# Kernel optimization log

Hardware: AMD Instinct MI355X
Metric: run time of the kernel (lower is better)

The kernel has to match this reference:

```python
import jax, jax.numpy as jnp
import numpy as np

K = 256  # number of leaf nodes in the cluster tree


def setup_inputs() -> dict:
    key = jax.random.key(0)
    k1, k2 = jax.random.split(key)
    minibatch = jax.random.normal(k1, (131072, 64), dtype=jnp.float32)
    centers = jax.random.normal(k2, (K, 64), dtype=jnp.float32)
    return {"minibatch": minibatch, "centers": centers}


def reference(minibatch, centers):
    # Euclidean cdist (p=2) between samples [N,D] and leaf centers [K,D]
    x_sq = jnp.sum(minibatch * minibatch, axis=1, keepdims=True)      # [N,1]
    c_sq = jnp.sum(centers * centers, axis=1)[None, :]                # [1,K]
    dist_sq = x_sq + c_sq - 2.0 * (minibatch @ centers.T)             # [N,K]
    dist_sq = jnp.maximum(dist_sq, 0.0)
    dist = jnp.sqrt(dist_sq)

    # nearest-leaf routing (torch.min over dim=1)
    assignments = jnp.argmin(dist, axis=1)                            # [N] int
    min_dists = jnp.min(dist, axis=1)                                 # [N]

    # per-leaf statistics (vectorized form of the per-node assignment loop):
    # counts -> node.assignments length, sums -> analytic center updates,
    # sum_sq -> node.sum_squared_dist
    ones = jnp.ones(minibatch.shape[0], dtype=minibatch.dtype)
    leaf_counts = jax.ops.segment_sum(ones, assignments, num_segments=K)           # [K]
    leaf_sums = jax.ops.segment_sum(minibatch, assignments, num_segments=K)        # [K,D]
    leaf_sum_sq_dist = jax.ops.segment_sum(min_dists * min_dists, assignments,
                                           num_segments=K)                         # [K]
    return assignments, min_dists, leaf_counts, leaf_sums, leaf_sum_sq_dist
```

## Files before the change

kernel.cpp:

```cpp
#include <hip/hip_runtime.h>
#include <float.h>

#define NS 131072
#define DD 64
#define KK 256
#define CPAD 72
#define NSTAT 16896
#define XTS 264
#define XTSW 132
#define NCOPY 512
#define RGROUPS 16
#define RPER 32
#define P_OFF_F ((size_t)NCOPY * NSTAT)
#define P_CSQ_F 9216
#define P_IMG_I4 2304

typedef __attribute__((ext_vector_type(8))) short bf16x8;
typedef __attribute__((ext_vector_type(4))) float f32x4;
typedef __attribute__((ext_vector_type(4))) unsigned int u32x4;


__global__ void zero_buf(float* __restrict__ p, int n) {
    int i = blockIdx.x * 256 + threadIdx.x;
    if (i < n) p[i] = 0.f;
}

__device__ inline unsigned short f2bf(float f) {
    unsigned u = __float_as_uint(f);
    u += 0x7FFFu + ((u >> 16) & 1u);
    return (unsigned short)(u >> 16);
}
__device__ inline float bf2f(unsigned short b) {
    return __uint_as_float(((unsigned)b) << 16);
}

__global__ void prep_centers(const float* __restrict__ ctr, float* __restrict__ P) {
    __shared__ float s_part[32][9];
    const int t = threadIdx.x;
    const int rl = t >> 3, seg = t & 7;
    const int r = blockIdx.x * 32 + rl;
    const float* rp = ctr + r * DD + seg * 8;
    float4 a = ((const float4*)rp)[0];
    float4 b = ((const float4*)rp)[1];
    unsigned short u0 = f2bf(a.x), u1 = f2bf(a.y), u2 = f2bf(a.z), u3 = f2bf(a.w);
    unsigned short u4 = f2bf(b.x), u5 = f2bf(b.y), u6 = f2bf(b.z), u7 = f2bf(b.w);
    float q0 = bf2f(u0), q1 = bf2f(u1), q2 = bf2f(u2), q3 = bf2f(u3);
    float q4 = bf2f(u4), q5 = bf2f(u5), q6 = bf2f(u6), q7 = bf2f(u7);
    float p = (q0*q0 + q1*q1 + q2*q2 + q3*q3) + (q4*q4 + q5*q5 + q6*q6 + q7*q7);

    unsigned short* Pu = (unsigned short*)P;
    int4 pack;
    pack.x = (int)((unsigned)u0 | ((unsigned)u1 << 16));
    pack.y = (int)((unsigned)u2 | ((unsigned)u3 << 16));
    pack.z = (int)((unsigned)u4 | ((unsigned)u5 << 16));
    pack.w = (int)((unsigned)u6 | ((unsigned)u7 << 16));
    *(int4*)(Pu + (size_t)r * CPAD + seg * 8) = pack;
    if (seg == 0) {
        int4 z; z.x = 0; z.y = 0; z.z = 0; z.w = 0;
        *(int4*)(Pu + (size_t)r * CPAD + 64) = z;
    }
    s_part[rl][seg] = p;
    __syncthreads();
    if (seg == 0) {
        float s = 0.f;
        #pragma unroll
        for (int k = 0; k < 8; ++k) s += s_part[rl][k];
        P[P_CSQ_F + r] = s;
    }
}

__global__ void reduce_ws1(float* __restrict__ ws) {
    int gid = blockIdx.x * 256 + threadIdx.x;
    if (gid >= NSTAT * RGROUPS) return;
    int g = gid / NSTAT, e = gid - g * NSTAT;
    const float* src = ws + (size_t)(g * RPER) * NSTAT + e;
    float s = 0.f;
    #pragma unroll 8
    for (int j = 0; j < RPER; ++j) s += src[(size_t)j * NSTAT];
    ws[(size_t)(g * RPER) * NSTAT + e] = s;
}

__global__ void reduce_ws2(const float* __restrict__ ws, float* __restrict__ o_stats) {
    int e = blockIdx.x * 256 + threadIdx.x;
    if (e >= NSTAT) return;
    float s = 0.f;
    #pragma unroll
    for (int g = 0; g < RGROUPS; ++g) s += ws[(size_t)(g * RPER) * NSTAT + e];
    int leaf = e / 66, c = e - leaf * 66;
    float* o_cnt = o_stats;
    float* o_sum = o_stats + KK;
    float* o_ssq = o_stats + KK + KK * DD;
    if (c < 64)       o_sum[leaf * 64 + c] = s;
    else if (c == 64) o_cnt[leaf] = s;
    else              o_ssq[leaf] = s;
}

__global__ __launch_bounds__(512, 2)
void deepect_fused(const float* __restrict__ mb, const float* __restrict__ P,
                   float* __restrict__ out, float* __restrict__ ws) {
    __shared__ __align__(16) unsigned short s_ctr[KK][CPAD];
    __shared__ float s_csq[KK];
    __shared__ __align__(16) unsigned short s_xt[64][XTS];
    __shared__ __align__(16) int s_bi[256];
    __shared__ float s_cnt[KK];
    __shared__ float s_ssq[KK];

    const int tid  = threadIdx.x;
    const int lane = tid & 63;
    const int w    = tid >> 6;
    const int g    = lane >> 4;
    const int c16  = lane & 15;
    const int base = blockIdx.x * 256;

    {
        const int4* Pi = (const int4*)P;
        for (int i = tid; i < P_IMG_I4; i += 512)
            ((int4*)s_ctr)[i] = Pi[i];
    }
    if (tid < KK) {
        s_csq[tid] = P[P_CSQ_F + tid];
        s_cnt[tid] = 0.f;
        s_ssq[tid] = 0.f;
    }

    {
        unsigned* xtw = (unsigned*)s_xt;
        const int dh = tid >> 7, sp = tid & 127;
        const float* r0 = mb + (size_t)(base + 2 * sp) * DD + dh * 16;
        const float* r1 = r0 + DD;
        #pragma unroll
        for (int q = 0; q < 4; ++q) {
            float4 a = ((const float4*)r0)[q];
            float4 b = ((const float4*)r1)[q];
            const int row = dh * 16 + q * 4;
            xtw[(row + 0) * XTSW + sp] = (unsigned)f2bf(a.x) | ((unsigned)f2bf(b.x) << 16);
            xtw[(row + 1) * XTSW + sp] = (unsigned)f2bf(a.y) | ((unsigned)f2bf(b.y) << 16);
            xtw[(row + 2) * XTSW + sp] = (unsigned)f2bf(a.z) | ((unsigned)f2bf(b.z) << 16);
            xtw[(row + 3) * XTSW + sp] = (unsigned)f2bf(a.w) | ((unsigned)f2bf(b.w) << 16);
        }
    }
    __syncthreads();

    float csqh[16];
    #pragma unroll
    for (int t = 0; t < 16; ++t) csqh[t] = -0.5f * s_csq[t * 16 + c16];

    const int sbase = base + w * 32;
    bf16x8 afr[2][2];
    float  xsq_rt[2];
    #pragma unroll
    for (int rt = 0; rt < 2; ++rt) {
        float px = 0.f;
        #pragma unroll
        for (int ks = 0; ks < 2; ++ks) {
            const float* rp = mb + (size_t)(sbase + rt * 16 + c16) * DD + g * 8 + ks * 32;
            float4 a = ((const float4*)rp)[0];
            float4 b = ((const float4*)rp)[1];
            bf16x8 f;
            f[0] = (short)f2bf(a.x); f[1] = (short)f2bf(a.y);
            f[2] = (short)f2bf(a.z); f[3] = (short)f2bf(a.w);
            f[4] = (short)f2bf(b.x); f[5] = (short)f2bf(b.y);
            f[6] = (short)f2bf(b.z); f[7] = (short)f2bf(b.w);
            afr[rt][ks] = f;
            float q0 = bf2f(f2bf(a.x)), q1 = bf2f(f2bf(a.y)), q2 = bf2f(f2bf(a.z)), q3 = bf2f(f2bf(a.w));
            float q4 = bf2f(f2bf(b.x)), q5 = bf2f(f2bf(b.y)), q6 = bf2f(f2bf(b.z)), q7 = bf2f(f2bf(b.w));
            px += q0*q0 + q1*q1 + q2*q2 + q3*q3 + q4*q4 + q5*q5 + q6*q6 + q7*q7;
        }
        px += __shfl_xor(px, 16, 64);
        px += __shfl_xor(px, 32, 64);
        xsq_rt[rt] = px;
    }

    float bestv[2][4];
    int   besti[2][4];
    #pragma unroll
    for (int rt = 0; rt < 2; ++rt)
        #pragma unroll
        for (int r = 0; r < 4; ++r) { bestv[rt][r] = -FLT_MAX; besti[rt][r] = 0; }

    #pragma unroll
    for (int t = 0; t < 16; ++t) {
        bf16x8 b0 = *(bf16x8*)&s_ctr[t * 16 + c16][g * 8];
        bf16x8 b1 = *(bf16x8*)&s_ctr[t * 16 + c16][g * 8 + 32];
        const int colidx = t * 16 + c16;
        #pragma unroll
        for (int rt = 0; rt < 2; ++rt) {
            f32x4 acc;
            acc[0] = csqh[t]; acc[1] = csqh[t]; acc[2] = csqh[t]; acc[3] = csqh[t];
            acc = __builtin_amdgcn_mfma_f32_16x16x32_bf16(afr[rt][0], b0, acc, 0, 0, 0);
            acc = __builtin_amdgcn_mfma_f32_16x16x32_bf16(afr[rt][1], b1, acc, 0, 0, 0);
            #pragma unroll
            for (int r = 0; r < 4; ++r) {
                if (acc[r] > bestv[rt][r]) { bestv[rt][r] = acc[r]; besti[rt][r] = colidx; }
            }
        }
    }

    float* o_assign = out;
    float* o_mind   = out + NS;

    #pragma unroll
    for (int rt = 0; rt < 2; ++rt) {
        #pragma unroll
        for (int r = 0; r < 4; ++r) {
            float v  = bestv[rt][r];
            int   bi = besti[rt][r];
            #pragma unroll
            for (int off = 1; off < 16; off <<= 1) {
                float ov = __shfl_xor(v, off, 64);
                int   oi = __shfl_xor(bi, off, 64);
                if (ov > v || (ov == v && oi < bi)) { v = ov; bi = oi; }
            }
            int src = (lane & 48) | (g * 4 + r);
            float xq = __shfl(xsq_rt[rt], src, 64);
            float dsq = fmaxf(xq - 2.0f * v, 0.f);
            if (c16 == 0) {
                const int lrow = w * 32 + rt * 16 + g * 4 + r;
                o_assign[base + lrow] = (float)bi;
                o_mind[base + lrow]   = sqrtf(dsq);
                s_bi[lrow] = bi;
                atomicAdd(&s_cnt[bi], 1.0f);
                atomicAdd(&s_ssq[bi], dsq);
            }
        }
    }
    __syncthreads();

    f32x4 acc[2][4];
    #pragma unroll
    for (int L = 0; L < 2; ++L)
        #pragma unroll
        for (int dt = 0; dt < 4; ++dt) {
            acc[L][dt][0] = 0.f; acc[L][dt][1] = 0.f;
            acc[L][dt][2] = 0.f; acc[L][dt][3] = 0.f;
        }

    const int ml0 = w * 16 + c16;
    const int ml1 = (w + 8) * 16 + c16;

    #pragma unroll
    for (int ks = 0; ks < 8; ++ks) {
        const int kb = ks * 32 + g * 8;
        int4 bl = *(int4*)&s_bi[kb];
        int4 bh = *(int4*)&s_bi[kb + 4];
        bf16x8 bfrag[4];
        #pragma unroll
        for (int dt = 0; dt < 4; ++dt)
            bfrag[dt] = *(bf16x8*)&s_xt[dt * 16 + c16][kb];

        const int b0 = bl.x, b1 = bl.y, b2 = bl.z, b3 = bl.w;
        const int b4 = bh.x, b5 = bh.y, b6 = bh.z, b7 = bh.w;
        u32x4 u0, u1;
        u0[0] = (b0 == ml0 ? 0x3F80u : 0u) | (b1 == ml0 ? 0x3F800000u : 0u);
        u0[1] = (b2 == ml0 ? 0x3F80u : 0u) | (b3 == ml0 ? 0x3F800000u : 0u);
        u0[2] = (b4 == ml0 ? 0x3F80u : 0u) | (b5 == ml0 ? 0x3F800000u : 0u);
        u0[3] = (b6 == ml0 ? 0x3F80u : 0u) | (b7 == ml0 ? 0x3F800000u : 0u);
        u1[0] = (b0 == ml1 ? 0x3F80u : 0u) | (b1 == ml1 ? 0x3F800000u : 0u);
        u1[1] = (b2 == ml1 ? 0x3F80u : 0u) | (b3 == ml1 ? 0x3F800000u : 0u);
        u1[2] = (b4 == ml1 ? 0x3F80u : 0u) | (b5 == ml1 ? 0x3F800000u : 0u);
        u1[3] = (b6 == ml1 ? 0x3F80u : 0u) | (b7 == ml1 ? 0x3F800000u : 0u);
        bf16x8 a0 = __builtin_bit_cast(bf16x8, u0);
        bf16x8 a1 = __builtin_bit_cast(bf16x8, u1);

        #pragma unroll
        for (int dt = 0; dt < 4; ++dt) {
            acc[0][dt] = __builtin_amdgcn_mfma_f32_16x16x32_bf16(a0, bfrag[dt], acc[0][dt], 0, 0, 0);
            acc[1][dt] = __builtin_amdgcn_mfma_f32_16x16x32_bf16(a1, bfrag[dt], acc[1][dt], 0, 0, 0);
        }
    }

    float* dst = ws + (size_t)blockIdx.x * NSTAT;
    #pragma unroll
    for (int L = 0; L < 2; ++L) {
        const int lt = (L == 0) ? w : (w + 8);
        #pragma unroll
        for (int dt = 0; dt < 4; ++dt) {
            const int col = dt * 16 + c16;
            #pragma unroll
            for (int r = 0; r < 4; ++r) {
                const int leaf = lt * 16 + g * 4 + r;
                dst[leaf * 66 + col] = acc[L][dt][r];
            }
        }
    }
    if (tid < KK) {
        dst[tid * 66 + 64] = s_cnt[tid];
        dst[tid * 66 + 65] = s_ssq[tid];
    }
}

__global__ __launch_bounds__(512, 2)
void deepect_argmin(const float* __restrict__ mb, const float* __restrict__ ctr,
                    float* __restrict__ out) {
    __shared__ __align__(16) unsigned short s_ctr[KK][CPAD];
    __shared__ float s_csq[KK];

    const int tid  = threadIdx.x;
    const int lane = tid & 63;
    const int w    = tid >> 6;
    const int g    = lane >> 4;
    const int c16  = lane & 15;

    for (int idx = tid; idx < KK * 16; idx += 512) {
        int row = idx >> 4, f4 = idx & 15;
        float4 v = ((const float4*)(ctr + row * DD))[f4];
        ushort4 b;
        b.x = f2bf(v.x); b.y = f2bf(v.y); b.z = f2bf(v.z); b.w = f2bf(v.w);
        *(ushort4*)&s_ctr[row][f4 * 4] = b;
    }
    __syncthreads();

    if (tid < KK) {
        float acc = 0.f;
        #pragma unroll
        for (int j = 0; j < 16; ++j) {
            ushort4 b = *(ushort4*)&s_ctr[tid][j * 4];
            float x0 = bf2f(b.x), x1 = bf2f(b.y), x2 = bf2f(b.z), x3 = bf2f(b.w);
            acc += x0 * x0 + x1 * x1 + x2 * x2 + x3 * x3;
        }
        s_csq[tid] = acc;
    }
    __syncthreads();

    float csqh[16];
    #pragma unroll
    for (int t = 0; t < 16; ++t) csqh[t] = -0.5f * s_csq[t * 16 + c16];

    const int sbase = blockIdx.x * 256 + w * 32;

    bf16x8 afr[2][2];
    float  xsq_rt[2];
    #pragma unroll
    for (int rt = 0; rt < 2; ++rt) {
        float px = 0.f;
        #pragma unroll
        for (int ks = 0; ks < 2; ++ks) {
            const float* rp = mb + (size_t)(sbase + rt * 16 + c16) * DD + g * 8 + ks * 32;
            float4 a = ((const float4*)rp)[0];
            float4 b = ((const float4*)rp)[1];
            bf16x8 f;
            f[0] = (short)f2bf(a.x); f[1] = (short)f2bf(a.y);
            f[2] = (short)f2bf(a.z); f[3] = (short)f2bf(a.w);
            f[4] = (short)f2bf(b.x); f[5] = (short)f2bf(b.y);
            f[6] = (short)f2bf(b.z); f[7] = (short)f2bf(b.w);
            afr[rt][ks] = f;
            float q0 = bf2f(f2bf(a.x)), q1 = bf2f(f2bf(a.y)), q2 = bf2f(f2bf(a.z)), q3 = bf2f(f2bf(a.w));
            float q4 = bf2f(f2bf(b.x)), q5 = bf2f(f2bf(b.y)), q6 = bf2f(f2bf(b.z)), q7 = bf2f(f2bf(b.w));
            px += q0*q0 + q1*q1 + q2*q2 + q3*q3 + q4*q4 + q5*q5 + q6*q6 + q7*q7;
        }
        px += __shfl_xor(px, 16, 64);
        px += __shfl_xor(px, 32, 64);
        xsq_rt[rt] = px;
    }

    float bestv[2][4];
    int   besti[2][4];
    #pragma unroll
    for (int rt = 0; rt < 2; ++rt)
        #pragma unroll
        for (int r = 0; r < 4; ++r) { bestv[rt][r] = -FLT_MAX; besti[rt][r] = 0; }

    #pragma unroll
    for (int t = 0; t < 16; ++t) {
        bf16x8 b0 = *(bf16x8*)&s_ctr[t * 16 + c16][g * 8];
        bf16x8 b1 = *(bf16x8*)&s_ctr[t * 16 + c16][g * 8 + 32];
        const int colidx = t * 16 + c16;
        #pragma unroll
        for (int rt = 0; rt < 2; ++rt) {
            f32x4 acc;
            acc[0] = csqh[t]; acc[1] = csqh[t]; acc[2] = csqh[t]; acc[3] = csqh[t];
            acc = __builtin_amdgcn_mfma_f32_16x16x32_bf16(afr[rt][0], b0, acc, 0, 0, 0);
            acc = __builtin_amdgcn_mfma_f32_16x16x32_bf16(afr[rt][1], b1, acc, 0, 0, 0);
            #pragma unroll
            for (int r = 0; r < 4; ++r) {
                if (acc[r] > bestv[rt][r]) { bestv[rt][r] = acc[r]; besti[rt][r] = colidx; }
            }
        }
    }

    float* o_assign = out;
    float* o_mind   = out + NS;

    #pragma unroll
    for (int rt = 0; rt < 2; ++rt) {
        #pragma unroll
        for (int r = 0; r < 4; ++r) {
            float v  = bestv[rt][r];
            int   bi = besti[rt][r];
            #pragma unroll
            for (int off = 1; off < 16; off <<= 1) {
                float ov = __shfl_xor(v, off, 64);
                int   oi = __shfl_xor(bi, off, 64);
                if (ov > v || (ov == v && oi < bi)) { v = ov; bi = oi; }
            }
            int src = (lane & 48) | (g * 4 + r);
            float xq = __shfl(xsq_rt[rt], src, 64);
            float dsq = fmaxf(xq - 2.0f * v, 0.f);
            if (c16 == 0) {
                int s = sbase + rt * 16 + g * 4 + r;
                o_assign[s] = (float)bi;
                o_mind[s]   = sqrtf(dsq);
            }
        }
    }
}

__global__ __launch_bounds__(512)
void deepect_stats_atomic(const float* __restrict__ mb, const float* __restrict__ out,
                          float* __restrict__ o_stats) {
    __shared__ float s_cnt[KK];
    __shared__ float s_ssq[KK];
    __shared__ float s_sum[KK][65];

    const int tid = threadIdx.x;
    for (int idx = tid; idx < KK; idx += 512) { s_cnt[idx] = 0.f; s_ssq[idx] = 0.f; }
    for (int idx = tid; idx < KK * 65; idx += 512) ((float*)s_sum)[idx] = 0.f;
    __syncthreads();

    const int grp = tid >> 4;
    const int d4  = tid & 15;
    const int ibase = blockIdx.x * 512 + grp * 16;

    for (int s = 0; s < 16; ++s) {
        const int i = ibase + s;
        const int bi = (int)out[i];
        float4 v = ((const float4*)(mb + (size_t)i * DD))[d4];
        atomicAdd(&s_sum[bi][d4 * 4 + 0], v.x);
        atomicAdd(&s_sum[bi][d4 * 4 + 1], v.y);
        atomicAdd(&s_sum[bi][d4 * 4 + 2], v.z);
        atomicAdd(&s_sum[bi][d4 * 4 + 3], v.w);
        if (d4 == 0) {
            const float md = out[NS + i];
            atomicAdd(&s_cnt[bi], 1.0f);
            atomicAdd(&s_ssq[bi], md * md);
        }
    }
    __syncthreads();

    for (int idx = tid; idx < KK; idx += 512) {
        atomicAdd(&o_stats[idx], s_cnt[idx]);
        atomicAdd(&o_stats[KK + KK * DD + idx], s_ssq[idx]);
    }
    for (int idx = tid; idx < KK * DD; idx += 512)
        atomicAdd(&o_stats[KK + idx], s_sum[idx >> 6][idx & 63]);
}

extern "C" void kernel_launch(void* const* d_in, const int* in_sizes, int n_in,
                              void* d_out, int out_size, void* d_ws, size_t ws_size,
                              hipStream_t stream) {
    const float* mb  = (const float*)d_in[0];
    const float* ctr = (const float*)d_in[1];
    float* out = (float*)d_out;
    float* o_stats = out + 2 * NS;
    float* ws = (float*)d_ws;

    const size_t need = (P_OFF_F + P_CSQ_F + KK) * sizeof(float);

    if (ws_size >= need) {
        float* P = ws + P_OFF_F;
        hipLaunchKernelGGL(prep_centers, dim3(8), dim3(256), 0, stream, ctr, P);
        hipLaunchKernelGGL(deepect_fused, dim3(NS / 256), dim3(512), 0, stream,
                           mb, P, out, ws);
        hipLaunchKernelGGL(reduce_ws1, dim3((NSTAT * RGROUPS + 255) / 256), dim3(256),
                           0, stream, ws);
        hipLaunchKernelGGL(reduce_ws2, dim3((NSTAT + 255) / 256), dim3(256), 0, stream,
                           ws, o_stats);
    } else {
        hipLaunchKernelGGL(zero_buf, dim3((NSTAT + 255) / 256), dim3(256), 0, stream,
                           o_stats, NSTAT);
        hipLaunchKernelGGL(deepect_argmin, dim3(NS / 256), dim3(512), 0, stream,
                           mb, ctr, out);
        hipLaunchKernelGGL(deepect_stats_atomic, dim3(NS / 512), dim3(512), 0, stream,
                           mb, out, o_stats);
    }
}
```

Measured before the change: 54.86 us.

## Split fused kernel into argmin and stats-GEMM kernels with bf16 partials

Splits the fused argmin+stats kernel into two kernels. The argmin kernel reads centers directly from global memory with smaller 256-thread blocks. The stats kernel folds counts and squared distances into the one-hot MFMA by adding a ones row and a min-dist-squared row. Per-block partial sums are now stored as bf16, halving the workspace traffic for the reduction. The trade-offs are a second full read of the minibatch, an extra launch, and lower precision in the accumulated statistics (counts and sums rounded to bf16 per block).

```diff
diff --git a/kernel.cpp b/kernel.cpp
--- a/kernel.cpp
+++ b/kernel.cpp
@@ -1,4 +1,5 @@
 #include <hip/hip_runtime.h>
+#include <hip/hip_bf16.h>
 #include <float.h>
 
 #define NS 131072
@@ -11,7 +12,8 @@
 #define NCOPY 512
 #define RGROUPS 16
 #define RPER 32
-#define P_OFF_F ((size_t)NCOPY * NSTAT)
+#define SCR_OFF_F ((size_t)NCOPY * NSTAT / 2)
+#define P_OFF_F   (SCR_OFF_F + (size_t)RGROUPS * NSTAT)
 #define P_CSQ_F 9216
 #define P_IMG_I4 2304
 
@@ -26,9 +28,9 @@
 }
 
 __device__ inline unsigned short f2bf(float f) {
-    unsigned u = __float_as_uint(f);
-    u += 0x7FFFu + ((u >> 16) & 1u);
-    return (unsigned short)(u >> 16);
+    union { __hip_bfloat16 h; unsigned short u; } v;
+    v.h = __float2bfloat16(f);
+    return v.u;
 }
 __device__ inline float bf2f(unsigned short b) {
     return __uint_as_float(((unsigned)b) << 16);
@@ -69,83 +71,25 @@
     }
 }
 
-__global__ void reduce_ws1(float* __restrict__ ws) {
-    int gid = blockIdx.x * 256 + threadIdx.x;
-    if (gid >= NSTAT * RGROUPS) return;
-    int g = gid / NSTAT, e = gid - g * NSTAT;
-    const float* src = ws + (size_t)(g * RPER) * NSTAT + e;
-    float s = 0.f;
-    #pragma unroll 8
-    for (int j = 0; j < RPER; ++j) s += src[(size_t)j * NSTAT];
-    ws[(size_t)(g * RPER) * NSTAT + e] = s;
-}
-
-__global__ void reduce_ws2(const float* __restrict__ ws, float* __restrict__ o_stats) {
-    int e = blockIdx.x * 256 + threadIdx.x;
-    if (e >= NSTAT) return;
-    float s = 0.f;
-    #pragma unroll
-    for (int g = 0; g < RGROUPS; ++g) s += ws[(size_t)(g * RPER) * NSTAT + e];
-    int leaf = e / 66, c = e - leaf * 66;
-    float* o_cnt = o_stats;
-    float* o_sum = o_stats + KK;
-    float* o_ssq = o_stats + KK + KK * DD;
-    if (c < 64)       o_sum[leaf * 64 + c] = s;
-    else if (c == 64) o_cnt[leaf] = s;
-    else              o_ssq[leaf] = s;
-}
-
-__global__ __launch_bounds__(512, 2)
-void deepect_fused(const float* __restrict__ mb, const float* __restrict__ P,
-                   float* __restrict__ out, float* __restrict__ ws) {
-    __shared__ __align__(16) unsigned short s_ctr[KK][CPAD];
+__global__ __launch_bounds__(256, 4)
+void deepect_argmin(const float* __restrict__ mb, const float* __restrict__ P,
+                    float* __restrict__ out) {
     __shared__ float s_csq[KK];
-    __shared__ __align__(16) unsigned short s_xt[64][XTS];
-    __shared__ __align__(16) int s_bi[256];
-    __shared__ float s_cnt[KK];
-    __shared__ float s_ssq[KK];
-
     const int tid  = threadIdx.x;
     const int lane = tid & 63;
     const int w    = tid >> 6;
     const int g    = lane >> 4;
     const int c16  = lane & 15;
-    const int base = blockIdx.x * 256;
-
-    {
-        const int4* Pi = (const int4*)P;
-        for (int i = tid; i < P_IMG_I4; i += 512)
-            ((int4*)s_ctr)[i] = Pi[i];
-    }
-    if (tid < KK) {
-        s_csq[tid] = P[P_CSQ_F + tid];
-        s_cnt[tid] = 0.f;
-        s_ssq[tid] = 0.f;
-    }
-
-    {
-        unsigned* xtw = (unsigned*)s_xt;
-        const int dh = tid >> 7, sp = tid & 127;
-        const float* r0 = mb + (size_t)(base + 2 * sp) * DD + dh * 16;
-        const float* r1 = r0 + DD;
-        #pragma unroll
-        for (int q = 0; q < 4; ++q) {
-            float4 a = ((const float4*)r0)[q];
-            float4 b = ((const float4*)r1)[q];
-            const int row = dh * 16 + q * 4;
-            xtw[(row + 0) * XTSW + sp] = (unsigned)f2bf(a.x) | ((unsigned)f2bf(b.x) << 16);
-            xtw[(row + 1) * XTSW + sp] = (unsigned)f2bf(a.y) | ((unsigned)f2bf(b.y) << 16);
-            xtw[(row + 2) * XTSW + sp] = (unsigned)f2bf(a.z) | ((unsigned)f2bf(b.z) << 16);
-            xtw[(row + 3) * XTSW + sp] = (unsigned)f2bf(a.w) | ((unsigned)f2bf(b.w) << 16);
-        }
-    }
+
+    if (tid < KK) s_csq[tid] = P[P_CSQ_F + tid];
     __syncthreads();
 
     float csqh[16];
     #pragma unroll
     for (int t = 0; t < 16; ++t) csqh[t] = -0.5f * s_csq[t * 16 + c16];
 
-    const int sbase = base + w * 32;
+    const int sbase = blockIdx.x * 128 + w * 32;
+
     bf16x8 afr[2][2];
     float  xsq_rt[2];
     #pragma unroll
@@ -162,9 +106,8 @@
             f[4] = (short)f2bf(b.x); f[5] = (short)f2bf(b.y);
             f[6] = (short)f2bf(b.z); f[7] = (short)f2bf(b.w);
             afr[rt][ks] = f;
-            float q0 = bf2f(f2bf(a.x)), q1 = bf2f(f2bf(a.y)), q2 = bf2f(f2bf(a.z)), q3 = bf2f(f2bf(a.w));
-            float q4 = bf2f(f2bf(b.x)), q5 = bf2f(f2bf(b.y)), q6 = bf2f(f2bf(b.z)), q7 = bf2f(f2bf(b.w));
-            px += q0*q0 + q1*q1 + q2*q2 + q3*q3 + q4*q4 + q5*q5 + q6*q6 + q7*q7;
+            px += a.x*a.x + a.y*a.y + a.z*a.z + a.w*a.w
+                + b.x*b.x + b.y*b.y + b.z*b.z + b.w*b.w;
         }
         px += __shfl_xor(px, 16, 64);
         px += __shfl_xor(px, 32, 64);
@@ -178,10 +121,11 @@
         #pragma unroll
         for (int r = 0; r < 4; ++r) { bestv[rt][r] = -FLT_MAX; besti[rt][r] = 0; }
 
+    const unsigned short* Pu = (const unsigned short*)P;
     #pragma unroll
     for (int t = 0; t < 16; ++t) {
-        bf16x8 b0 = *(bf16x8*)&s_ctr[t * 16 + c16][g * 8];
-        bf16x8 b1 = *(bf16x8*)&s_ctr[t * 16 + c16][g * 8 + 32];
+        const bf16x8 b0 = *(const bf16x8*)(Pu + (size_t)(t * 16 + c16) * CPAD + g * 8);
+        const bf16x8 b1 = *(const bf16x8*)(Pu + (size_t)(t * 16 + c16) * CPAD + g * 8 + 32);
         const int colidx = t * 16 + c16;
         #pragma unroll
         for (int rt = 0; rt < 2; ++rt) {
@@ -215,22 +159,61 @@
             float xq = __shfl(xsq_rt[rt], src, 64);
             float dsq = fmaxf(xq - 2.0f * v, 0.f);
             if (c16 == 0) {
-                const int lrow = w * 32 + rt * 16 + g * 4 + r;
-                o_assign[base + lrow] = (float)bi;
-                o_mind[base + lrow]   = sqrtf(dsq);
-                s_bi[lrow] = bi;
-                atomicAdd(&s_cnt[bi], 1.0f);
-                atomicAdd(&s_ssq[bi], dsq);
-            }
-        }
-    }
-    __syncthreads();
-
-    f32x4 acc[2][4];
+                int s = sbase + rt * 16 + g * 4 + r;
+                o_assign[s] = (float)bi;
+                o_mind[s]   = sqrtf(dsq);
+            }
+        }
+    }
+}
+
+__global__ __launch_bounds__(512, 2)
+void deepect_stats_gemm(const float* __restrict__ mb, const float* __restrict__ out,
+                        float* __restrict__ ws) {
+    __shared__ __align__(16) unsigned short s_xt[80][XTS];
+    __shared__ int s_bi[256];
+
+    const int tid  = threadIdx.x;
+    const int lane = tid & 63;
+    const int w    = tid >> 6;
+    const int g    = lane >> 4;
+    const int c16  = lane & 15;
+    const int base = blockIdx.x * 256;
+
+    unsigned* xtw = (unsigned*)s_xt;
+
+    for (int i = tid; i < 14 * XTSW; i += 512) xtw[66 * XTSW + i] = 0u;
+
+    {
+        const int dh = tid >> 7, sp = tid & 127;
+        const float* r0 = mb + (size_t)(base + 2 * sp) * DD + dh * 16;
+        const float* r1 = r0 + DD;
+        #pragma unroll
+        for (int q = 0; q < 4; ++q) {
+            float4 a = ((const float4*)r0)[q];
+            float4 b = ((const float4*)r1)[q];
+            const int row = dh * 16 + q * 4;
+            xtw[(row + 0) * XTSW + sp] = (unsigned)f2bf(a.x) | ((unsigned)f2bf(b.x) << 16);
+            xtw[(row + 1) * XTSW + sp] = (unsigned)f2bf(a.y) | ((unsigned)f2bf(b.y) << 16);
+            xtw[(row + 2) * XTSW + sp] = (unsigned)f2bf(a.z) | ((unsigned)f2bf(b.z) << 16);
+            xtw[(row + 3) * XTSW + sp] = (unsigned)f2bf(a.w) | ((unsigned)f2bf(b.w) << 16);
+        }
+    }
+    if (tid < 128) {
+        const int sp = tid;
+        float m0 = out[NS + base + 2 * sp];
+        float m1 = out[NS + base + 2 * sp + 1];
+        xtw[64 * XTSW + sp] = 0x3F803F80u;
+        xtw[65 * XTSW + sp] = (unsigned)f2bf(m0 * m0) | ((unsigned)f2bf(m1 * m1) << 16);
+    }
+    if (tid < 256) s_bi[tid] = (int)out[base + tid];
+    __syncthreads();
+
+    f32x4 acc[2][5];
     #pragma unroll
     for (int L = 0; L < 2; ++L)
         #pragma unroll
-        for (int dt = 0; dt < 4; ++dt) {
+        for (int dt = 0; dt < 5; ++dt) {
             acc[L][dt][0] = 0.f; acc[L][dt][1] = 0.f;
             acc[L][dt][2] = 0.f; acc[L][dt][3] = 0.f;
         }
@@ -243,9 +226,9 @@
         const int kb = ks * 32 + g * 8;
         int4 bl = *(int4*)&s_bi[kb];
         int4 bh = *(int4*)&s_bi[kb + 4];
-        bf16x8 bfrag[4];
-        #pragma unroll
-        for (int dt = 0; dt < 4; ++dt)
+        bf16x8 bfrag[5];
+        #pragma unroll
+        for (int dt = 0; dt < 5; ++dt)
             bfrag[dt] = *(bf16x8*)&s_xt[dt * 16 + c16][kb];
 
         const int b0 = bl.x, b1 = bl.y, b2 = bl.z, b3 = bl.w;
@@ -263,35 +246,57 @@
         bf16x8 a1 = __builtin_bit_cast(bf16x8, u1);
 
         #pragma unroll
-        for (int dt = 0; dt < 4; ++dt) {
+        for (int dt = 0; dt < 5; ++dt) {
             acc[0][dt] = __builtin_amdgcn_mfma_f32_16x16x32_bf16(a0, bfrag[dt], acc[0][dt], 0, 0, 0);
             acc[1][dt] = __builtin_amdgcn_mfma_f32_16x16x32_bf16(a1, bfrag[dt], acc[1][dt], 0, 0, 0);
         }
     }
 
-    float* dst = ws + (size_t)blockIdx.x * NSTAT;
+    unsigned short* dstu = (unsigned short*)ws + (size_t)blockIdx.x * NSTAT;
     #pragma unroll
     for (int L = 0; L < 2; ++L) {
         const int lt = (L == 0) ? w : (w + 8);
         #pragma unroll
-        for (int dt = 0; dt < 4; ++dt) {
+        for (int dt = 0; dt < 5; ++dt) {
             const int col = dt * 16 + c16;
             #pragma unroll
             for (int r = 0; r < 4; ++r) {
                 const int leaf = lt * 16 + g * 4 + r;
-                dst[leaf * 66 + col] = acc[L][dt][r];
-            }
-        }
-    }
-    if (tid < KK) {
-        dst[tid * 66 + 64] = s_cnt[tid];
-        dst[tid * 66 + 65] = s_ssq[tid];
-    }
+                if (col < 66) dstu[leaf * 66 + col] = f2bf(acc[L][dt][r]);
+            }
+        }
+    }
+}
+
+__global__ void reduce_ws1(float* __restrict__ ws) {
+    int gid = blockIdx.x * 256 + threadIdx.x;
+    if (gid >= NSTAT * RGROUPS) return;
+    int g = gid / NSTAT, e = gid - g * NSTAT;
+    const unsigned short* src = (const unsigned short*)ws + (size_t)(g * RPER) * NSTAT + e;
+    float s = 0.f;
+    #pragma unroll 8
+    for (int j = 0; j < RPER; ++j) s += bf2f(src[(size_t)j * NSTAT]);
+    ws[SCR_OFF_F + (size_t)g * NSTAT + e] = s;
+}
+
+__global__ void reduce_ws2(const float* __restrict__ ws, float* __restrict__ o_stats) {
+    int e = blockIdx.x * 256 + threadIdx.x;
+    if (e >= NSTAT) return;
+    float s = 0.f;
+    #pragma unroll
+    for (int g = 0; g < RGROUPS; ++g) s += ws[SCR_OFF_F + (size_t)g * NSTAT + e];
+    int leaf = e / 66, c = e - leaf * 66;
+    float* o_cnt = o_stats;
+    float* o_sum = o_stats + KK;
+    float* o_ssq = o_stats + KK + KK * DD;
+    if (c < 64)       o_sum[leaf * 64 + c] = s;
+    else if (c == 64) o_cnt[leaf] = s;
+    else              o_ssq[leaf] = s;
 }
 
 __global__ __launch_bounds__(512, 2)
-void deepect_argmin(const float* __restrict__ mb, const float* __restrict__ ctr,
-                    float* __restrict__ out) {
+void deepect_argmin_fb(const float* __restrict__ mb, const float* __restrict__ ctr,
+                       float* __restrict__ out) {
     __shared__ __align__(16) unsigned short s_ctr[KK][CPAD];
     __shared__ float s_csq[KK];
 
@@ -344,9 +349,8 @@
             f[4] = (short)f2bf(b.x); f[5] = (short)f2bf(b.y);
             f[6] = (short)f2bf(b.z); f[7] = (short)f2bf(b.w);
             afr[rt][ks] = f;
-            float q0 = bf2f(f2bf(a.x)), q1 = bf2f(f2bf(a.y)), q2 = bf2f(f2bf(a.z)), q3 = bf2f(f2bf(a.w));
-            float q4 = bf2f(f2bf(b.x)), q5 = bf2f(f2bf(b.y)), q6 = bf2f(f2bf(b.z)), q7 = bf2f(f2bf(b.w));
-            px += q0*q0 + q1*q1 + q2*q2 + q3*q3 + q4*q4 + q5*q5 + q6*q6 + q7*q7;
+            px += a.x*a.x + a.y*a.y + a.z*a.z + a.w*a.w
+                + b.x*b.x + b.y*b.y + b.z*b.z + b.w*b.w;
         }
         px += __shfl_xor(px, 16, 64);
         px += __shfl_xor(px, 32, 64);
@@ -459,8 +463,10 @@
     if (ws_size >= need) {
         float* P = ws + P_OFF_F;
         hipLaunchKernelGGL(prep_centers, dim3(8), dim3(256), 0, stream, ctr, P);
-        hipLaunchKernelGGL(deepect_fused, dim3(NS / 256), dim3(512), 0, stream,
-                           mb, P, out, ws);
+        hipLaunchKernelGGL(deepect_argmin, dim3(NS / 128), dim3(256), 0, stream,
+                           mb, P, out);
+        hipLaunchKernelGGL(deepect_stats_gemm, dim3(NS / 256), dim3(512), 0, stream,
+                           mb, out, ws);
         hipLaunchKernelGGL(reduce_ws1, dim3((NSTAT * RGROUPS + 255) / 256), dim3(256),
                            0, stream, ws);
         hipLaunchKernelGGL(reduce_ws2, dim3((NSTAT + 255) / 256), dim3(256), 0, stream,
@@ -468,7 +474,7 @@
     } else {
         hipLaunchKernelGGL(zero_buf, dim3((NSTAT + 255) / 256), dim3(256), 0, stream,
                            o_stats, NSTAT);
-        hipLaunchKernelGGL(deepect_argmin, dim3(NS / 256), dim3(512), 0, stream,
+        hipLaunchKernelGGL(deepect_argmin_fb, dim3(NS / 256), dim3(512), 0, stream,
                            mb, ctr, out);
         hipLaunchKernelGGL(deepect_stats_atomic, dim3(NS / 512), dim3(512), 0, stream,
                            mb, out, o_stats);
```

After: 63.53 us. 15.8% more time.
